# Kernel tuning notes

Measured on AMD Instinct MI355X. Metric: run time of the kernel, lower is better.

## Reference

```python
import jax, jax.numpy as jnp
import numpy as np
from jax.scipy.special import xlogy

N = 8192
NUM_CLASSES = 100

def setup_inputs() -> dict:
    key = jax.random.key(0)
    k1, k2, k3 = jax.random.split(key, 3)
    pred1 = jax.random.normal(k1, (N, N), dtype=jnp.float32)
    pred2 = jax.random.normal(k2, (N, N), dtype=jnp.float32)
    labels = jax.random.randint(k3, (N,), 0, NUM_CLASSES, dtype=jnp.int64)
    return {"pred1": pred1, "pred2": pred2, "labels": labels}

def _kl_div_mean(log_input, target):
    # torch.nn.KLDivLoss(reduction='mean'): mean over ALL elements of
    # target * (log(target) - log_input), with 0*log(0) := 0 (xlogy).
    return jnp.mean(xlogy(target, target) - target * log_input)

def reference(pred1, pred2, labels):
    n = pred1.shape[0]
    # vectorized replacement of the python double loop: gt[i,k] = (labels[k]==labels[i])
    gt = (labels[None, :] == labels[:, None]).astype(pred1.dtype)
    probs3 = jax.nn.softmax(gt * 10.0, axis=1)  # [N,N] soft target rows
    logp1 = jax.nn.log_softmax(pred1, axis=1)
    logp2 = jax.nn.log_softmax(pred2, axis=1)
    loss1 = _kl_div_mean(logp1, probs3) * n
    loss2 = _kl_div_mean(logp2, probs3.T) * n
    return (loss1 + loss2) / 2.0
```

## Files before the change

### kernel.cpp

```cpp
#include <hip/hip_runtime.h>
#include <math.h>


constexpr int N_ = 8192;
constexpr int NCLS = 100;
constexpr float E10F = 22026.465794806718f;

__global__ void prep_kernel(const int* __restrict__ labels,
                            int* __restrict__ counts,
                            float* __restrict__ wcls,
                            float* __restrict__ Wout,
                            float* __restrict__ warr) {
    __shared__ int cnt[NCLS];
    __shared__ float wsh[NCLS];
    int tid = threadIdx.x;
    if (tid < NCLS) cnt[tid] = 0;
    __syncthreads();
    for (int i = tid; i < N_; i += blockDim.x)
        atomicAdd(&cnt[labels[i]], 1);
    __syncthreads();
    if (tid < NCLS) {
        int c = cnt[tid];
        counts[tid] = c;
        float D = (float)c * E10F + (float)(N_ - c);
        float w = 1.0f / D;
        wcls[tid] = w;
        wsh[tid] = w;
    }
    __syncthreads();
    for (int i = tid; i < N_; i += blockDim.x)
        warr[i] = wsh[labels[i]];
    if (tid == 0) {
        double W = 0.0;
        const double e10 = 22026.465794806718;
        for (int c = 0; c < NCLS; ++c) {
            double cc = (double)cnt[c];
            double D = cc * e10 + ((double)N_ - cc);
            W += cc / D;
        }
        Wout[0] = (float)W;
    }
}

template <bool SECOND>
__device__ __forceinline__ void row_body(const float4* __restrict__ row4,
                                         const int4* __restrict__ lab4,
                                         const float4* __restrict__ w4p,
                                         int rowlab,
                                         float& m, float& s, float& sum, float& msum) {
#pragma unroll
    for (int it = 0; it < 8; ++it) {
        const int idx = it * 256 + (int)threadIdx.x;
        float4 v = row4[idx];
        int4 lb = lab4[idx];

        float vmax = fmaxf(fmaxf(v.x, v.y), fmaxf(v.z, v.w));
        float nm = fmaxf(m, vmax);
        s = s * __expf(m - nm) + __expf(v.x - nm) + __expf(v.y - nm) +
            __expf(v.z - nm) + __expf(v.w - nm);
        m = nm;

        if (SECOND) {
            float4 w = w4p[idx];
            sum = fmaf(v.x, w.x, fmaf(v.y, w.y, fmaf(v.z, w.z, fmaf(v.w, w.w, sum))));
        } else {
            sum += (v.x + v.y) + (v.z + v.w);
        }
        msum += (lb.x == rowlab ? v.x : 0.0f) + (lb.y == rowlab ? v.y : 0.0f) +
                (lb.z == rowlab ? v.z : 0.0f) + (lb.w == rowlab ? v.w : 0.0f);
    }
}

__launch_bounds__(256)
__global__ void row_kernel(const float* __restrict__ pred1,
                           const float* __restrict__ pred2,
                           const int* __restrict__ labels,
                           const float* __restrict__ warr,
                           const int* __restrict__ counts,
                           const float* __restrict__ wcls,
                           const float* __restrict__ Wptr,
                           float* __restrict__ contrib) {
    const int bid = blockIdx.x;
    const int which = bid & 1;
    const int r = bid >> 1;
    const int tid = threadIdx.x;
    const float* pred = which ? pred2 : pred1;
    const float4* row4 = reinterpret_cast<const float4*>(pred + (size_t)r * N_);
    const int4* lab4 = reinterpret_cast<const int4*>(labels);
    const float4* w4p = reinterpret_cast<const float4*>(warr);
    const int rowlab = labels[r];

    float m = -1e30f, s = 0.0f, sum = 0.0f, msum = 0.0f;
    if (which == 0)
        row_body<false>(row4, lab4, w4p, rowlab, m, s, sum, msum);
    else
        row_body<true>(row4, lab4, w4p, rowlab, m, s, sum, msum);

#pragma unroll
    for (int mask = 32; mask >= 1; mask >>= 1) {
        float om = __shfl_xor(m, mask, 64);
        float os = __shfl_xor(s, mask, 64);
        float nm = fmaxf(m, om);
        s = s * __expf(m - nm) + os * __expf(om - nm);
        m = nm;
        sum += __shfl_xor(sum, mask, 64);
        msum += __shfl_xor(msum, mask, 64);
    }

    __shared__ float redm[4], reds[4], redsum[4], redmsum[4];
    const int wave = tid >> 6;
    if ((tid & 63) == 0) {
        redm[wave] = m; reds[wave] = s; redsum[wave] = sum; redmsum[wave] = msum;
    }
    __syncthreads();
    if (tid == 0) {
        float M = redm[0], S = reds[0], SU = redsum[0], MS = redmsum[0];
#pragma unroll
        for (int wv = 1; wv < 4; ++wv) {
            float om = redm[wv], os = reds[wv];
            float nm = fmaxf(M, om);
            S = S * __expf(M - nm) + os * __expf(om - nm);
            M = nm;
            SU += redsum[wv];
            MS += redmsum[wv];
        }
        float lse = logf(S) + M;
        int cnt = counts[rowlab];
        float w = wcls[rowlab];
        float c;
        if (which == 0) {
            c = w * (SU - (float)N_ * lse) + (E10F - 1.0f) * w * (MS - (float)cnt * lse);
        } else {
            float W = Wptr[0];
            c = (SU - lse * W) + (E10F - 1.0f) * w * (MS - (float)cnt * lse);
        }
        contrib[which * N_ + r] = c;
    }
}

__global__ void final_kernel(const int* __restrict__ counts,
                             const float* __restrict__ contrib,
                             float* __restrict__ out) {
    __shared__ double red[256];
    int tid = threadIdx.x;
    double acc = 0.0;
    for (int i = tid; i < 2 * N_; i += 256)
        acc += (double)contrib[i];
    red[tid] = acc;
    __syncthreads();
    for (int st = 128; st > 0; st >>= 1) {
        if (tid < st) red[tid] += red[tid + st];
        __syncthreads();
    }
    if (tid == 0) {
        const double e10 = 22026.465794806718;
        double H = 0.0;
        for (int c = 0; c < NCLS; ++c) {
            double cc = (double)counts[c];
            double D = cc * e10 + ((double)N_ - cc);
            double logD = log(D);
            H += cc * (cc * (e10 / D) * (10.0 - logD) +
                       ((double)N_ - cc) * (1.0 / D) * (-logD));
        }
        out[0] = (float)((2.0 * H - red[0]) / (2.0 * (double)N_));
    }
}

extern "C" void kernel_launch(void* const* d_in, const int* in_sizes, int n_in,
                              void* d_out, int out_size, void* d_ws, size_t ws_size,
                              hipStream_t stream) {
    const float* pred1 = (const float*)d_in[0];
    const float* pred2 = (const float*)d_in[1];
    const int* labels = (const int*)d_in[2];
    float* out = (float*)d_out;

    float* wsf = (float*)d_ws;
    int* wsi = (int*)d_ws;
    int* counts   = wsi;
    float* wcls   = wsf + 128;
    float* Wptr   = wsf + 256;
    float* warr   = wsf + 512;
    float* contrib = wsf + 8704;

    prep_kernel<<<1, 1024, 0, stream>>>(labels, counts, wcls, Wptr, warr);
    row_kernel<<<2 * N_, 256, 0, stream>>>(pred1, pred2, labels, warr,
                                           counts, wcls, Wptr, contrib);
    final_kernel<<<1, 256, 0, stream>>>(counts, contrib, out);
}
```

Measured before the change: 174.7 us.

## Process both prediction rows per block with two-pass register-resident softmax

Each block now handles row r of both pred1 and pred2, loading all 16 float4 values per thread into registers up front, then computing the max first and a plain exp-sum second instead of an online softmax. This halves the grid, shares the label and weight loads between the two matrices, issues more loads in flight per thread, and removes the per-iteration rescale exponentials. In exchange register pressure rises, which may lower occupancy.

```diff
diff --git a/kernel.cpp b/kernel.cpp
--- a/kernel.cpp
+++ b/kernel.cpp
@@ -42,35 +42,6 @@
     }
 }
 
-template <bool SECOND>
-__device__ __forceinline__ void row_body(const float4* __restrict__ row4,
-                                         const int4* __restrict__ lab4,
-                                         const float4* __restrict__ w4p,
-                                         int rowlab,
-                                         float& m, float& s, float& sum, float& msum) {
-#pragma unroll
-    for (int it = 0; it < 8; ++it) {
-        const int idx = it * 256 + (int)threadIdx.x;
-        float4 v = row4[idx];
-        int4 lb = lab4[idx];
-
-        float vmax = fmaxf(fmaxf(v.x, v.y), fmaxf(v.z, v.w));
-        float nm = fmaxf(m, vmax);
-        s = s * __expf(m - nm) + __expf(v.x - nm) + __expf(v.y - nm) +
-            __expf(v.z - nm) + __expf(v.w - nm);
-        m = nm;
-
-        if (SECOND) {
-            float4 w = w4p[idx];
-            sum = fmaf(v.x, w.x, fmaf(v.y, w.y, fmaf(v.z, w.z, fmaf(v.w, w.w, sum))));
-        } else {
-            sum += (v.x + v.y) + (v.z + v.w);
-        }
-        msum += (lb.x == rowlab ? v.x : 0.0f) + (lb.y == rowlab ? v.y : 0.0f) +
-                (lb.z == rowlab ? v.z : 0.0f) + (lb.w == rowlab ? v.w : 0.0f);
-    }
-}
-
 __launch_bounds__(256)
 __global__ void row_kernel(const float* __restrict__ pred1,
                            const float* __restrict__ pred2,
@@ -80,61 +51,91 @@
                            const float* __restrict__ wcls,
                            const float* __restrict__ Wptr,
                            float* __restrict__ contrib) {
-    const int bid = blockIdx.x;
-    const int which = bid & 1;
-    const int r = bid >> 1;
+    const int r = blockIdx.x;
     const int tid = threadIdx.x;
-    const float* pred = which ? pred2 : pred1;
-    const float4* row4 = reinterpret_cast<const float4*>(pred + (size_t)r * N_);
+    const float4* row1 = reinterpret_cast<const float4*>(pred1 + (size_t)r * N_);
+    const float4* row2 = reinterpret_cast<const float4*>(pred2 + (size_t)r * N_);
     const int4* lab4 = reinterpret_cast<const int4*>(labels);
     const float4* w4p = reinterpret_cast<const float4*>(warr);
     const int rowlab = labels[r];
 
-    float m = -1e30f, s = 0.0f, sum = 0.0f, msum = 0.0f;
-    if (which == 0)
-        row_body<false>(row4, lab4, w4p, rowlab, m, s, sum, msum);
-    else
-        row_body<true>(row4, lab4, w4p, rowlab, m, s, sum, msum);
+    float4 a[8], b[8];
+#pragma unroll
+    for (int it = 0; it < 8; ++it) a[it] = row1[it * 256 + tid];
+#pragma unroll
+    for (int it = 0; it < 8; ++it) b[it] = row2[it * 256 + tid];
+
+    float m1 = -1e30f, m2 = -1e30f;
+#pragma unroll
+    for (int it = 0; it < 8; ++it) {
+        m1 = fmaxf(m1, fmaxf(fmaxf(a[it].x, a[it].y), fmaxf(a[it].z, a[it].w)));
+        m2 = fmaxf(m2, fmaxf(fmaxf(b[it].x, b[it].y), fmaxf(b[it].z, b[it].w)));
+    }
+
+    float s1 = 0.f, s2 = 0.f, sum1 = 0.f, sum2 = 0.f, ms1 = 0.f, ms2 = 0.f;
+#pragma unroll
+    for (int it = 0; it < 8; ++it) {
+        const int idx = it * 256 + tid;
+        int4 lb = lab4[idx];
+        float4 w = w4p[idx];
+        float4 v = a[it];
+        s1 += __expf(v.x - m1) + __expf(v.y - m1) + __expf(v.z - m1) + __expf(v.w - m1);
+        sum1 += (v.x + v.y) + (v.z + v.w);
+        ms1 += (lb.x == rowlab ? v.x : 0.f) + (lb.y == rowlab ? v.y : 0.f) +
+               (lb.z == rowlab ? v.z : 0.f) + (lb.w == rowlab ? v.w : 0.f);
+        float4 u = b[it];
+        s2 += __expf(u.x - m2) + __expf(u.y - m2) + __expf(u.z - m2) + __expf(u.w - m2);
+        sum2 = fmaf(u.x, w.x, fmaf(u.y, w.y, fmaf(u.z, w.z, fmaf(u.w, w.w, sum2))));
+        ms2 += (lb.x == rowlab ? u.x : 0.f) + (lb.y == rowlab ? u.y : 0.f) +
+               (lb.z == rowlab ? u.z : 0.f) + (lb.w == rowlab ? u.w : 0.f);
+    }
 
 #pragma unroll
     for (int mask = 32; mask >= 1; mask >>= 1) {
-        float om = __shfl_xor(m, mask, 64);
-        float os = __shfl_xor(s, mask, 64);
-        float nm = fmaxf(m, om);
-        s = s * __expf(m - nm) + os * __expf(om - nm);
-        m = nm;
-        sum += __shfl_xor(sum, mask, 64);
-        msum += __shfl_xor(msum, mask, 64);
+        float om1 = __shfl_xor(m1, mask, 64), os1 = __shfl_xor(s1, mask, 64);
+        float nm1 = fmaxf(m1, om1);
+        s1 = s1 * __expf(m1 - nm1) + os1 * __expf(om1 - nm1);
+        m1 = nm1;
+        float om2 = __shfl_xor(m2, mask, 64), os2 = __shfl_xor(s2, mask, 64);
+        float nm2 = fmaxf(m2, om2);
+        s2 = s2 * __expf(m2 - nm2) + os2 * __expf(om2 - nm2);
+        m2 = nm2;
+        sum1 += __shfl_xor(sum1, mask, 64);
+        sum2 += __shfl_xor(sum2, mask, 64);
+        ms1 += __shfl_xor(ms1, mask, 64);
+        ms2 += __shfl_xor(ms2, mask, 64);
     }
 
-    __shared__ float redm[4], reds[4], redsum[4], redmsum[4];
+    __shared__ float rm1[4], rs1[4], rsu1[4], rms1[4], rm2[4], rs2[4], rsu2[4], rms2[4];
     const int wave = tid >> 6;
     if ((tid & 63) == 0) {
-        redm[wave] = m; reds[wave] = s; redsum[wave] = sum; redmsum[wave] = msum;
+        rm1[wave] = m1; rs1[wave] = s1; rsu1[wave] = sum1; rms1[wave] = ms1;
+        rm2[wave] = m2; rs2[wave] = s2; rsu2[wave] = sum2; rms2[wave] = ms2;
     }
     __syncthreads();
     if (tid == 0) {
-        float M = redm[0], S = reds[0], SU = redsum[0], MS = redmsum[0];
+        float M1 = rm1[0], S1 = rs1[0], SU1 = rsu1[0], MS1 = rms1[0];
+        float M2 = rm2[0], S2 = rs2[0], SU2 = rsu2[0], MS2 = rms2[0];
 #pragma unroll
         for (int wv = 1; wv < 4; ++wv) {
-            float om = redm[wv], os = reds[wv];
-            float nm = fmaxf(M, om);
-            S = S * __expf(M - nm) + os * __expf(om - nm);
-            M = nm;
-            SU += redsum[wv];
-            MS += redmsum[wv];
+            float om = rm1[wv], os = rs1[wv];
+            float nm = fmaxf(M1, om);
+            S1 = S1 * __expf(M1 - nm) + os * __expf(om - nm);
+            M1 = nm; SU1 += rsu1[wv]; MS1 += rms1[wv];
+            om = rm2[wv]; os = rs2[wv];
+            nm = fmaxf(M2, om);
+            S2 = S2 * __expf(M2 - nm) + os * __expf(om - nm);
+            M2 = nm; SU2 += rsu2[wv]; MS2 += rms2[wv];
         }
-        float lse = logf(S) + M;
+        float lse1 = logf(S1) + M1;
+        float lse2 = logf(S2) + M2;
         int cnt = counts[rowlab];
         float w = wcls[rowlab];
-        float c;
-        if (which == 0) {
-            c = w * (SU - (float)N_ * lse) + (E10F - 1.0f) * w * (MS - (float)cnt * lse);
-        } else {
-            float W = Wptr[0];
-            c = (SU - lse * W) + (E10F - 1.0f) * w * (MS - (float)cnt * lse);
-        }
-        contrib[which * N_ + r] = c;
+        float W = Wptr[0];
+        contrib[r] = w * (SU1 - (float)N_ * lse1) +
+                     (E10F - 1.0f) * w * (MS1 - (float)cnt * lse1);
+        contrib[N_ + r] = (SU2 - lse2 * W) +
+                          (E10F - 1.0f) * w * (MS2 - (float)cnt * lse2);
     }
 }
 
@@ -183,7 +184,7 @@
     float* contrib = wsf + 8704;
 
     prep_kernel<<<1, 1024, 0, stream>>>(labels, counts, wcls, Wptr, warr);
-    row_kernel<<<2 * N_, 256, 0, stream>>>(pred1, pred2, labels, warr,
-                                           counts, wcls, Wptr, contrib);
+    row_kernel<<<N_, 256, 0, stream>>>(pred1, pred2, labels, warr,
+                                       counts, wcls, Wptr, contrib);
     final_kernel<<<1, 256, 0, stream>>>(counts, contrib, out);
 }
```

New measurement: 152.6 us. 1.14x faster.
